# Performance work log

Measured on AMD Instinct MI355X. Metric: run time of the kernel, lower is better.

Reference implementation:

```python
import jax, jax.numpy as jnp
import numpy as np

B, N, IN_F, OUT_F = 32, 1024, 256, 256
ALPHA = 0.2  # LeakyReLU negative slope
NEG_INF = -9e15  # matches torch's -9000000000000000.0 masking constant


def setup_inputs() -> dict:
    key = jax.random.key(0)
    k1, k2, k3, k4 = jax.random.split(key, 4)
    h = jax.random.normal(k1, (B, N, IN_F), dtype=jnp.float32)
    adj = jax.random.randint(k2, (B, N, N), 0, 2, dtype=jnp.int32)
    W = jax.random.normal(k3, (OUT_F, IN_F), dtype=jnp.float32) * 0.05
    a = jax.random.normal(k4, (1, 2 * OUT_F), dtype=jnp.float32) * 0.05
    return {"h": h, "adj": adj, "W": W, "a": a}


def reference(h, adj, W, a):
    # Wh: (B, N, out)
    Wh = jnp.einsum("bni,oi->bno", h, W)
    # Decompose a([Wh_i || Wh_j]) = Wh_i . a1 + Wh_j . a2 (identical math,
    # avoids the O(B*N^2*2*out) concat intermediate of the torch code).
    a1 = a[0, :OUT_F]   # (out,)
    a2 = a[0, OUT_F:]   # (out,)
    si = Wh @ a1        # (B, N) score contribution of source node i
    sj = Wh @ a2        # (B, N) score contribution of neighbor node j
    e = jax.nn.leaky_relu(si[:, :, None] + sj[:, None, :], negative_slope=ALPHA)
    attention = jnp.where(adj > 0, e, NEG_INF)
    attention = jax.nn.softmax(attention, axis=-1)
    # dropout omitted (eval mode)
    h_prime = jnp.einsum("bij,bjo->bio", attention, Wh)
    return jax.nn.elu(h_prime)
```

## Files before the change

### kernel.cpp

```cpp
#include <hip/hip_runtime.h>
#include <hip/hip_bf16.h>


#define ALPHA 0.2f
#define LOG2E 1.44269504f

typedef __bf16 bf16x8 __attribute__((ext_vector_type(8)));
typedef __bf16 bf16x4 __attribute__((ext_vector_type(4)));
typedef float  f32x4  __attribute__((ext_vector_type(4)));
typedef unsigned long long u64;

__global__ __launch_bounds__(256) void k1_gemm1(const float* __restrict__ h,
                                                const float* __restrict__ W,
                                                const float* __restrict__ a_g,
                                                __bf16* __restrict__ whT,
                                                float* __restrict__ si,
                                                float* __restrict__ sj) {
    __shared__ __bf16 hA[64 * 72];
    __shared__ __bf16 hB[256 * 72];
    __shared__ float  red[512];
    const int t    = threadIdx.x;
    const int r0   = blockIdx.x * 64;
    const int b    = r0 >> 10;
    const int n0   = r0 & 1023;
    const int w    = t >> 6;
    const int l    = t & 63;
    const int ln   = l & 15;
    const int quad = l >> 4;

    f32x4 acc[4][4] = {};
    float4 ha_r[4], wb_r[16];

    #pragma unroll
    for (int it = 0; it < 4; ++it)
        ha_r[it] = *(const float4*)&h[(size_t)(r0 + it * 16 + (t >> 4)) * 256 + (t & 15) * 4];
    #pragma unroll
    for (int it = 0; it < 16; ++it)
        wb_r[it] = *(const float4*)&W[(size_t)(it * 16 + (t >> 4)) * 256 + (t & 15) * 4];

    for (int kc = 0; kc < 4; ++kc) {
        #pragma unroll
        for (int it = 0; it < 4; ++it) {
            const float4 v = ha_r[it];
            bf16x4 pv = {(__bf16)v.x, (__bf16)v.y, (__bf16)v.z, (__bf16)v.w};
            *(bf16x4*)&hA[(it * 16 + (t >> 4)) * 72 + (t & 15) * 4] = pv;
        }
        #pragma unroll
        for (int it = 0; it < 16; ++it) {
            const float4 v = wb_r[it];
            bf16x4 pv = {(__bf16)v.x, (__bf16)v.y, (__bf16)v.z, (__bf16)v.w};
            *(bf16x4*)&hB[(it * 16 + (t >> 4)) * 72 + (t & 15) * 4] = pv;
        }
        __syncthreads();
        if (kc < 3) {
            const int k0 = (kc + 1) * 64;
            #pragma unroll
            for (int it = 0; it < 4; ++it)
                ha_r[it] = *(const float4*)&h[(size_t)(r0 + it * 16 + (t >> 4)) * 256 + k0 + (t & 15) * 4];
            #pragma unroll
            for (int it = 0; it < 16; ++it)
                wb_r[it] = *(const float4*)&W[(size_t)(it * 16 + (t >> 4)) * 256 + k0 + (t & 15) * 4];
        }
        #pragma unroll
        for (int kk = 0; kk < 2; ++kk) {
            bf16x8 af[4], bfr[4];
            #pragma unroll
            for (int ri = 0; ri < 4; ++ri)
                af[ri] = *(const bf16x8*)&hA[(ri * 16 + ln) * 72 + kk * 32 + quad * 8];
            #pragma unroll
            for (int oi = 0; oi < 4; ++oi)
                bfr[oi] = *(const bf16x8*)&hB[(w * 64 + oi * 16 + ln) * 72 + kk * 32 + quad * 8];
            #pragma unroll
            for (int ri = 0; ri < 4; ++ri)
                #pragma unroll
                for (int oi = 0; oi < 4; ++oi)
                    acc[ri][oi] = __builtin_amdgcn_mfma_f32_16x16x32_bf16(
                        af[ri], bfr[oi], acc[ri][oi], 0, 0, 0);
        }
        __syncthreads();
    }

    #pragma unroll
    for (int ri = 0; ri < 4; ++ri) {
        const int n = ri * 16 + quad * 4;
        #pragma unroll
        for (int oi = 0; oi < 4; ++oi) {
            const int o = w * 64 + oi * 16 + ln;
            bf16x4 pv = {(__bf16)acc[ri][oi][0], (__bf16)acc[ri][oi][1],
                         (__bf16)acc[ri][oi][2], (__bf16)acc[ri][oi][3]};
            *(bf16x4*)&hB[o * 72 + n] = pv;
        }
    }
    __syncthreads();

    #pragma unroll
    for (int it = 0; it < 8; ++it) {
        const int o   = w * 64 + it * 8 + (l >> 3);
        const int seg = l & 7;
        const bf16x8 v = *(const bf16x8*)&hB[o * 72 + seg * 8];
        *(bf16x8*)&whT[((size_t)b * 256 + o) * 1024 + n0 + seg * 8] = v;
    }

    {
        float s1 = 0.f, s2 = 0.f;
        #pragma unroll 8
        for (int oi = 0; oi < 64; ++oi) {
            const int o = w * 64 + oi;
            const float v = (float)hB[o * 72 + l];
            s1 += v * a_g[o];
            s2 += v * a_g[256 + o];
        }
        red[w * 64 + l]       = s1;
        red[256 + w * 64 + l] = s2;
    }
    __syncthreads();
    if (t < 64) {
        si[b * 1024 + n0 + t] =
            (red[t] + red[64 + t] + red[128 + t] + red[192 + t]) * LOG2E;
    } else if (t < 128) {
        const int n = t - 64;
        sj[b * 1024 + n0 + n] =
            (red[256 + n] + red[320 + n] + red[384 + n] + red[448 + n]) * LOG2E;
    }
}


#define SVAL(SI, SJE, AV) \
    ({ float _e = (SI) + (SJE); _e = fmaxf(_e, ALPHA * _e); \
       (AV) > 0 ? exp2f(_e) : 0.f; })

#define K3_BODY(J, A0, A1, B0, B1, SJ0, SJ1, NA0, NA1, NB0, NB1, NSJ0, NSJ1)   \
  {                                                                            \
    const int j0 = (J) * 32;                                                   \
        \
              \
                                                 \
    bf16x8 bfr[8];                                                             \
    _Pragma("unroll")                                                          \
    for (int oi = 0; oi < 8; ++oi)                                             \
      bfr[oi] = *(const bf16x8*)&whTb[                                         \
          (size_t)(oc + oi * 16 + ln) * 1024 + j0 + quad * 8];                 \
                               \
    if ((J) < 31) {                                                            \
      NA0 = *(const int4*)&adjw[(size_t)ln * 1024 + j0 + 32 + quad * 8];       \
      NA1 = *(const int4*)&adjw[(size_t)ln * 1024 + j0 + 32 + quad * 8 + 4];   \
      NB0 = *(const int4*)&adjw[(size_t)(ln + 16) * 1024 + j0 + 32 + quad * 8];\
      NB1 = *(const int4*)&adjw[(size_t)(ln + 16) * 1024 + j0 + 32 + quad * 8 + 4]; \
      NSJ0 = *(const float4*)&sj_g[bs + j0 + 32 + quad * 8];                   \
      NSJ1 = *(const float4*)&sj_g[bs + j0 + 32 + quad * 8 + 4];               \
    }                                                                          \
      \
    bf16x8 af0, af1;                                                           \
    af0[0] = (__bf16)SVAL(si0, SJ0.x, A0.x);                                   \
    af0[1] = (__bf16)SVAL(si0, SJ0.y, A0.y);                                   \
    af0[2] = (__bf16)SVAL(si0, SJ0.z, A0.z);                                   \
    af0[3] = (__bf16)SVAL(si0, SJ0.w, A0.w);                                   \
    af0[4] = (__bf16)SVAL(si0, SJ1.x, A1.x);                                   \
    af0[5] = (__bf16)SVAL(si0, SJ1.y, A1.y);                                   \
    af0[6] = (__bf16)SVAL(si0, SJ1.z, A1.z);                                   \
    af0[7] = (__bf16)SVAL(si0, SJ1.w, A1.w);                                   \
    af1[0] = (__bf16)SVAL(si1, SJ0.x, B0.x);                                   \
    af1[1] = (__bf16)SVAL(si1, SJ0.y, B0.y);                                   \
    af1[2] = (__bf16)SVAL(si1, SJ0.z, B0.z);                                   \
    af1[3] = (__bf16)SVAL(si1, SJ0.w, B0.w);                                   \
    af1[4] = (__bf16)SVAL(si1, SJ1.x, B1.x);                                   \
    af1[5] = (__bf16)SVAL(si1, SJ1.y, B1.y);                                   \
    af1[6] = (__bf16)SVAL(si1, SJ1.z, B1.z);                                   \
    af1[7] = (__bf16)SVAL(si1, SJ1.w, B1.w);                                   \
    dsum0 += (float)af0[0] + (float)af0[1] + (float)af0[2] + (float)af0[3]     \
           + (float)af0[4] + (float)af0[5] + (float)af0[6] + (float)af0[7];    \
    dsum1 += (float)af1[0] + (float)af1[1] + (float)af1[2] + (float)af1[3]     \
           + (float)af1[4] + (float)af1[5] + (float)af1[6] + (float)af1[7];    \
                                                \
    __builtin_amdgcn_s_setprio(1);                                             \
    _Pragma("unroll")                                                          \
    for (int oi = 0; oi < 8; ++oi) {                                           \
      acc0[oi] = __builtin_amdgcn_mfma_f32_16x16x32_bf16(af0, bfr[oi],         \
                                                         acc0[oi], 0, 0, 0);   \
      acc1[oi] = __builtin_amdgcn_mfma_f32_16x16x32_bf16(af1, bfr[oi],         \
                                                         acc1[oi], 0, 0, 0);   \
    }                                                                          \
    __builtin_amdgcn_s_setprio(0);                                             \
  }

__global__ __launch_bounds__(256, 2) void k3_attn(const int* __restrict__ adj,
                                                  const __bf16* __restrict__ whT,
                                                  const float* __restrict__ si_g,
                                                  const float* __restrict__ sj_g,
                                                  float* __restrict__ out) {
    const int t = threadIdx.x;
    const int orig = blockIdx.x;
    const int wgid = (orig & 7) * 64 + (orig >> 3);
    const int b    = wgid >> 4;
    const int i0   = (wgid & 15) << 6;
    const int w    = t >> 6;
    const int wr   = w >> 1;
    const int oc   = (w & 1) * 128;
    const int l    = t & 63;
    const int ln   = l & 15;
    const int quad = l >> 4;
    const int bs   = b * 1024;

    const __bf16* whTb = whT + (size_t)b * 256 * 1024;
    const int*    adjw = adj + ((size_t)(bs + i0 + wr * 32)) * 1024;

    const float si0 = si_g[bs + i0 + wr * 32 + ln];
    const float si1 = si_g[bs + i0 + wr * 32 + 16 + ln];

    float dsum0 = 0.f, dsum1 = 0.f;
    f32x4 acc0[8] = {}, acc1[8] = {};

    int4   a0_c, a1_c, b0_c, b1_c, a0_n, a1_n, b0_n, b1_n;
    float4 sj0_c, sj1_c, sj0_n, sj1_n;
    a0_c  = *(const int4*)&adjw[(size_t)ln * 1024 + quad * 8];
    a1_c  = *(const int4*)&adjw[(size_t)ln * 1024 + quad * 8 + 4];
    b0_c  = *(const int4*)&adjw[(size_t)(ln + 16) * 1024 + quad * 8];
    b1_c  = *(const int4*)&adjw[(size_t)(ln + 16) * 1024 + quad * 8 + 4];
    sj0_c = *(const float4*)&sj_g[bs + quad * 8];
    sj1_c = *(const float4*)&sj_g[bs + quad * 8 + 4];

    for (int jj = 0; jj < 16; ++jj) {
        K3_BODY(2 * jj,     a0_c, a1_c, b0_c, b1_c, sj0_c, sj1_c,
                            a0_n, a1_n, b0_n, b1_n, sj0_n, sj1_n);
        K3_BODY(2 * jj + 1, a0_n, a1_n, b0_n, b1_n, sj0_n, sj1_n,
                            a0_c, a1_c, b0_c, b1_c, sj0_c, sj1_c);
    }

    float d0 = dsum0; d0 += __shfl_xor(d0, 16); d0 += __shfl_xor(d0, 32);
    float d1 = dsum1; d1 += __shfl_xor(d1, 16); d1 += __shfl_xor(d1, 32);

    const int rbase = bs + i0 + wr * 32;
    #pragma unroll
    for (int q = 0; q < 4; ++q) {
        const int   rloc = quad * 4 + q;
        const float inv0 = 1.0f / fmaxf(__shfl(d0, rloc), 1e-30f);
        const float inv1 = 1.0f / fmaxf(__shfl(d1, rloc), 1e-30f);
        #pragma unroll
        for (int oi = 0; oi < 8; ++oi) {
            float v0 = acc0[oi][q] * inv0;
            v0 = v0 > 0.f ? v0 : __expf(v0) - 1.f;
            out[(size_t)(rbase + rloc) * 256 + oc + oi * 16 + ln] = v0;
            float v1 = acc1[oi][q] * inv1;
            v1 = v1 > 0.f ? v1 : __expf(v1) - 1.f;
            out[(size_t)(rbase + 16 + rloc) * 256 + oc + oi * 16 + ln] = v1;
        }
    }
}

extern "C" void kernel_launch(void* const* d_in, const int* in_sizes, int n_in,
                              void* d_out, int out_size, void* d_ws, size_t ws_size,
                              hipStream_t stream) {
    const float* h   = (const float*)d_in[0];
    const int*   adj = (const int*)d_in[1];
    const float* W   = (const float*)d_in[2];
    const float* a   = (const float*)d_in[3];
    float* out = (float*)d_out;

    __bf16* whT = (__bf16*)d_ws;
    float*  si  = (float*)((char*)d_ws + (size_t)16777216);
    float*  sj  = (float*)((char*)d_ws + (size_t)16777216 + 131072);

    k1_gemm1<<<512, 256, 0, stream>>>(h, W, a, whT, si, sj);
    k3_attn<<<512, 256, 0, stream>>>(adj, whT, si, sj, out);
}
```

Measured before the change: 303.7 us.

## Stage chunked WhT tiles through double-buffered LDS and compute each attention score once

Wh^T is now written in 32-column chunk-major layout. The attention kernel loads each 32x256 chunk cooperatively into double-buffered LDS, overlapping the next chunk's global load with the MFMAs on the current one. Each wave now owns 16 rows across all 256 output columns, so every exp score is computed once. Before, two waves each recomputed the scores for their output-column half and fetched B operands straight from global memory. The cost is a barrier per chunk, more accumulator registers (16 f32x4), and removal of the 2-blocks-per-CU launch bound, which may lower occupancy.

Measured after the change: 254.7 us. 16.1% less time.

```diff
diff --git a/kernel.cpp b/kernel.cpp
--- a/kernel.cpp
+++ b/kernel.cpp
@@ -98,7 +98,8 @@
         const int o   = w * 64 + it * 8 + (l >> 3);
         const int seg = l & 7;
         const bf16x8 v = *(const bf16x8*)&hB[o * 72 + seg * 8];
-        *(bf16x8*)&whT[((size_t)b * 256 + o) * 1024 + n0 + seg * 8] = v;
+        const int j   = n0 + seg * 8;
+        *(bf16x8*)&whT[(((size_t)b * 32 + (j >> 5)) * 256 + o) * 32 + (j & 31)] = v;
     }
 
     {
@@ -124,125 +125,130 @@
     }
 }
 
-
 #define SVAL(SI, SJE, AV) \
     ({ float _e = (SI) + (SJE); _e = fmaxf(_e, ALPHA * _e); \
        (AV) > 0 ? exp2f(_e) : 0.f; })
 
-#define K3_BODY(J, A0, A1, B0, B1, SJ0, SJ1, NA0, NA1, NB0, NB1, NSJ0, NSJ1)   \
+#define K3_CHUNK(C, BUFR, BUFW, AP0, AP1, SJ0, SJ1)                            \
   {                                                                            \
-    const int j0 = (J) * 32;                                                   \
-        \
-              \
-                                                 \
-    bf16x8 bfr[8];                                                             \
-    _Pragma("unroll")                                                          \
-    for (int oi = 0; oi < 8; ++oi)                                             \
-      bfr[oi] = *(const bf16x8*)&whTb[                                         \
-          (size_t)(oc + oi * 16 + ln) * 1024 + j0 + quad * 8];                 \
-                               \
-    if ((J) < 31) {                                                            \
-      NA0 = *(const int4*)&adjw[(size_t)ln * 1024 + j0 + 32 + quad * 8];       \
-      NA1 = *(const int4*)&adjw[(size_t)ln * 1024 + j0 + 32 + quad * 8 + 4];   \
-      NB0 = *(const int4*)&adjw[(size_t)(ln + 16) * 1024 + j0 + 32 + quad * 8];\
-      NB1 = *(const int4*)&adjw[(size_t)(ln + 16) * 1024 + j0 + 32 + quad * 8 + 4]; \
-      NSJ0 = *(const float4*)&sj_g[bs + j0 + 32 + quad * 8];                   \
-      NSJ1 = *(const float4*)&sj_g[bs + j0 + 32 + quad * 8 + 4];               \
-    }                                                                          \
-      \
-    bf16x8 af0, af1;                                                           \
-    af0[0] = (__bf16)SVAL(si0, SJ0.x, A0.x);                                   \
-    af0[1] = (__bf16)SVAL(si0, SJ0.y, A0.y);                                   \
-    af0[2] = (__bf16)SVAL(si0, SJ0.z, A0.z);                                   \
-    af0[3] = (__bf16)SVAL(si0, SJ0.w, A0.w);                                   \
-    af0[4] = (__bf16)SVAL(si0, SJ1.x, A1.x);                                   \
-    af0[5] = (__bf16)SVAL(si0, SJ1.y, A1.y);                                   \
-    af0[6] = (__bf16)SVAL(si0, SJ1.z, A1.z);                                   \
-    af0[7] = (__bf16)SVAL(si0, SJ1.w, A1.w);                                   \
-    af1[0] = (__bf16)SVAL(si1, SJ0.x, B0.x);                                   \
-    af1[1] = (__bf16)SVAL(si1, SJ0.y, B0.y);                                   \
-    af1[2] = (__bf16)SVAL(si1, SJ0.z, B0.z);                                   \
-    af1[3] = (__bf16)SVAL(si1, SJ0.w, B0.w);                                   \
-    af1[4] = (__bf16)SVAL(si1, SJ1.x, B1.x);                                   \
-    af1[5] = (__bf16)SVAL(si1, SJ1.y, B1.y);                                   \
-    af1[6] = (__bf16)SVAL(si1, SJ1.z, B1.z);                                   \
-    af1[7] = (__bf16)SVAL(si1, SJ1.w, B1.w);                                   \
-    dsum0 += (float)af0[0] + (float)af0[1] + (float)af0[2] + (float)af0[3]     \
-           + (float)af0[4] + (float)af0[5] + (float)af0[6] + (float)af0[7];    \
-    dsum1 += (float)af1[0] + (float)af1[1] + (float)af1[2] + (float)af1[3]     \
-           + (float)af1[4] + (float)af1[5] + (float)af1[6] + (float)af1[7];    \
-                                                \
+    const int c_ = (C);                                                        \
+           \
+    if (c_ < 31) {                                                             \
+      const __bf16* src = whTb + (size_t)(c_ + 1) * 8192;                      \
+      _Pragma("unroll")                                                        \
+      for (int p = 0; p < 4; ++p)                                              \
+        vs[p] = *(const bf16x8*)&src[p * 2048 + t * 8];                        \
+    }                                                                          \
+             \
+    bf16x8 af;                                                                 \
+    af[0] = (__bf16)SVAL(si0, SJ0.x, AP0.x);                                   \
+    af[1] = (__bf16)SVAL(si0, SJ0.y, AP0.y);                                   \
+    af[2] = (__bf16)SVAL(si0, SJ0.z, AP0.z);                                   \
+    af[3] = (__bf16)SVAL(si0, SJ0.w, AP0.w);                                   \
+    af[4] = (__bf16)SVAL(si0, SJ1.x, AP1.x);                                   \
+    af[5] = (__bf16)SVAL(si0, SJ1.y, AP1.y);                                   \
+    af[6] = (__bf16)SVAL(si0, SJ1.z, AP1.z);                                   \
+    af[7] = (__bf16)SVAL(si0, SJ1.w, AP1.w);                                   \
+    dsum += (float)af[0] + (float)af[1] + (float)af[2] + (float)af[3]          \
+          + (float)af[4] + (float)af[5] + (float)af[6] + (float)af[7];         \
+          \
+    if (c_ + 2 < 32) {                                                         \
+      const int jr = (c_ + 2) * 32 + quad * 8;                                 \
+      AP0 = *(const int4*)&adjb[arow + jr];                                    \
+      AP1 = *(const int4*)&adjb[arow + jr + 4];                                \
+      SJ0 = *(const float4*)&sjb[jr];                                          \
+      SJ1 = *(const float4*)&sjb[jr + 4];                                      \
+    }                                                                          \
+                           \
     __builtin_amdgcn_s_setprio(1);                                             \
     _Pragma("unroll")                                                          \
-    for (int oi = 0; oi < 8; ++oi) {                                           \
-      acc0[oi] = __builtin_amdgcn_mfma_f32_16x16x32_bf16(af0, bfr[oi],         \
-                                                         acc0[oi], 0, 0, 0);   \
-      acc1[oi] = __builtin_amdgcn_mfma_f32_16x16x32_bf16(af1, bfr[oi],         \
-                                                         acc1[oi], 0, 0, 0);   \
+    for (int oi = 0; oi < 16; ++oi) {                                          \
+      const bf16x8 bfr = *(const bf16x8*)&BUFR[(oi * 16 + ln) * 32 + quad * 8];\
+      acc[oi] = __builtin_amdgcn_mfma_f32_16x16x32_bf16(af, bfr, acc[oi],      \
+                                                        0, 0, 0);              \
     }                                                                          \
     __builtin_amdgcn_s_setprio(0);                                             \
+                           \
+    if (c_ < 31) {                                                             \
+      _Pragma("unroll")                                                        \
+      for (int p = 0; p < 4; ++p)                                              \
+        *(bf16x8*)&BUFW[p * 2048 + t * 8] = vs[p];                             \
+    }                                                                          \
+     \
+                     \
+    asm volatile("s_waitcnt lgkmcnt(0)" ::: "memory");                         \
+    __builtin_amdgcn_s_barrier();                                              \
   }
 
-__global__ __launch_bounds__(256, 2) void k3_attn(const int* __restrict__ adj,
-                                                  const __bf16* __restrict__ whT,
-                                                  const float* __restrict__ si_g,
-                                                  const float* __restrict__ sj_g,
-                                                  float* __restrict__ out) {
+__global__ __launch_bounds__(256) void k3_attn(const int* __restrict__ adj,
+                                               const __bf16* __restrict__ whT,
+                                               const float* __restrict__ si_g,
+                                               const float* __restrict__ sj_g,
+                                               float* __restrict__ out) {
+    __shared__ __bf16 bufA[8192];
+    __shared__ __bf16 bufB[8192];
+    __shared__ float  lds_denom[64];
     const int t = threadIdx.x;
     const int orig = blockIdx.x;
     const int wgid = (orig & 7) * 64 + (orig >> 3);
     const int b    = wgid >> 4;
     const int i0   = (wgid & 15) << 6;
     const int w    = t >> 6;
-    const int wr   = w >> 1;
-    const int oc   = (w & 1) * 128;
     const int l    = t & 63;
     const int ln   = l & 15;
     const int quad = l >> 4;
     const int bs   = b * 1024;
 
-    const __bf16* whTb = whT + (size_t)b * 256 * 1024;
-    const int*    adjw = adj + ((size_t)(bs + i0 + wr * 32)) * 1024;
-
-    const float si0 = si_g[bs + i0 + wr * 32 + ln];
-    const float si1 = si_g[bs + i0 + wr * 32 + 16 + ln];
-
-    float dsum0 = 0.f, dsum1 = 0.f;
-    f32x4 acc0[8] = {}, acc1[8] = {};
-
-    int4   a0_c, a1_c, b0_c, b1_c, a0_n, a1_n, b0_n, b1_n;
-    float4 sj0_c, sj1_c, sj0_n, sj1_n;
-    a0_c  = *(const int4*)&adjw[(size_t)ln * 1024 + quad * 8];
-    a1_c  = *(const int4*)&adjw[(size_t)ln * 1024 + quad * 8 + 4];
-    b0_c  = *(const int4*)&adjw[(size_t)(ln + 16) * 1024 + quad * 8];
-    b1_c  = *(const int4*)&adjw[(size_t)(ln + 16) * 1024 + quad * 8 + 4];
-    sj0_c = *(const float4*)&sj_g[bs + quad * 8];
-    sj1_c = *(const float4*)&sj_g[bs + quad * 8 + 4];
-
-    for (int jj = 0; jj < 16; ++jj) {
-        K3_BODY(2 * jj,     a0_c, a1_c, b0_c, b1_c, sj0_c, sj1_c,
-                            a0_n, a1_n, b0_n, b1_n, sj0_n, sj1_n);
-        K3_BODY(2 * jj + 1, a0_n, a1_n, b0_n, b1_n, sj0_n, sj1_n,
-                            a0_c, a1_c, b0_c, b1_c, sj0_c, sj1_c);
-    }
-
-    float d0 = dsum0; d0 += __shfl_xor(d0, 16); d0 += __shfl_xor(d0, 32);
-    float d1 = dsum1; d1 += __shfl_xor(d1, 16); d1 += __shfl_xor(d1, 32);
-
-    const int rbase = bs + i0 + wr * 32;
+    const __bf16* whTb = whT + (size_t)b * 32 * 8192;
+    const int*    adjb = adj + ((size_t)(bs + i0)) * 1024;
+    const float*  sjb  = sj_g + bs;
+    const size_t  arow = (size_t)(w * 16 + ln) * 1024;
+
+    const float si0 = si_g[bs + i0 + w * 16 + ln];
+
+    float dsum = 0.f;
+    f32x4 acc[16] = {};
+    bf16x8 vs[4];
+
+    #pragma unroll
+    for (int p = 0; p < 4; ++p)
+        vs[p] = *(const bf16x8*)&whTb[p * 2048 + t * 8];
+    #pragma unroll
+    for (int p = 0; p < 4; ++p)
+        *(bf16x8*)&bufA[p * 2048 + t * 8] = vs[p];
+
+    int4   a00, a01, a10, a11;
+    float4 s00, s01, s10, s11;
+    a00 = *(const int4*)&adjb[arow + quad * 8];
+    a01 = *(const int4*)&adjb[arow + quad * 8 + 4];
+    s00 = *(const float4*)&sjb[quad * 8];
+    s01 = *(const float4*)&sjb[quad * 8 + 4];
+    a10 = *(const int4*)&adjb[arow + 32 + quad * 8];
+    a11 = *(const int4*)&adjb[arow + 32 + quad * 8 + 4];
+    s10 = *(const float4*)&sjb[32 + quad * 8];
+    s11 = *(const float4*)&sjb[32 + quad * 8 + 4];
+    __syncthreads();
+
+    for (int cc = 0; cc < 16; ++cc) {
+        K3_CHUNK(2 * cc,     bufA, bufB, a00, a01, s00, s01);
+        K3_CHUNK(2 * cc + 1, bufB, bufA, a10, a11, s10, s11);
+    }
+
+    float d = dsum;
+    d += __shfl_xor(d, 16);
+    d += __shfl_xor(d, 32);
+    if (l < 16) lds_denom[w * 16 + l] = d;
+    __syncthreads();
+
     #pragma unroll
     for (int q = 0; q < 4; ++q) {
-        const int   rloc = quad * 4 + q;
-        const float inv0 = 1.0f / fmaxf(__shfl(d0, rloc), 1e-30f);
-        const float inv1 = 1.0f / fmaxf(__shfl(d1, rloc), 1e-30f);
-        #pragma unroll
-        for (int oi = 0; oi < 8; ++oi) {
-            float v0 = acc0[oi][q] * inv0;
-            v0 = v0 > 0.f ? v0 : __expf(v0) - 1.f;
-            out[(size_t)(rbase + rloc) * 256 + oc + oi * 16 + ln] = v0;
-            float v1 = acc1[oi][q] * inv1;
-            v1 = v1 > 0.f ? v1 : __expf(v1) - 1.f;
-            out[(size_t)(rbase + 16 + rloc) * 256 + oc + oi * 16 + ln] = v1;
+        const int row  = w * 16 + quad * 4 + q;
+        const float dinv = 1.0f / fmaxf(lds_denom[row], 1e-30f);
+        #pragma unroll
+        for (int oi = 0; oi < 16; ++oi) {
+            const float v = acc[oi][q] * dinv;
+            const float r = v > 0.f ? v : __expf(v) - 1.f;
+            out[((size_t)(bs + i0 + row)) * 256 + oi * 16 + ln] = r;
         }
     }
 }
```
